# Kernel optimization log

Hardware: AMD Instinct MI355X
Metric: run time of the kernel (lower is better)

Reference implementation:

```python
import jax, jax.numpy as jnp
import numpy as np
from jax import lax

D = 1024      # dim
E = 2         # expand
DI = D * E    # d_inner = 2048
DS = 16       # d_state
DK = 3        # d_conv (3 so padding=1 preserves seq length)
DTR = 64      # dt_rank = ceil(dim/16)
B = 2
L = 4096


def setup_inputs() -> dict:
    key = jax.random.key(0)
    ks = jax.random.split(key, 8)
    s = 0.02
    return {
        "x": jax.random.normal(ks[0], (B, L, D), jnp.float32),
        "W_in": jax.random.normal(ks[1], (D, 2 * DI), jnp.float32) * s,
        "W_conv": jax.random.normal(ks[2], (DI, 1, DK), jnp.float32) * s,
        "W_xproj": jax.random.normal(ks[3], (DI, DTR + 2 * DS), jnp.float32) * s,
        "W_dt": jax.random.normal(ks[4], (DTR, DI), jnp.float32) * s,
        "b_dt": jax.random.normal(ks[5], (DI,), jnp.float32) * s,
        "W_out": jax.random.normal(ks[6], (DI, D), jnp.float32) * s,
        "ln_g": jnp.ones((DI,), jnp.float32),
        "ln_b": jnp.zeros((DI,), jnp.float32),
    }


def _silu(v):
    return v * jax.nn.sigmoid(v)


def _forward(x, W_in, W_conv, W_xproj, W_dt, b_dt, W_out, ln_g, ln_b):
    # in_proj and gate split
    xz = x @ W_in                                   # (B,L,2*DI)
    xs, z = jnp.split(xz, 2, axis=-1)               # (B,L,DI) each
    # depthwise conv1d (groups = DI), padding preserves L
    xc = lax.conv_general_dilated(
        xs.transpose(0, 2, 1), W_conv, (1,), [(DK // 2, DK // 2)],
        dimension_numbers=("NCH", "OIH", "NCH"), feature_group_count=DI)
    xs = _silu(xc.transpose(0, 2, 1))               # (B,L,DI)
    # x_proj -> dt, B, C
    xp = xs @ W_xproj                               # (B,L,DTR+2*DS)
    dt_lo = xp[..., :DTR]
    Bp = xp[..., DTR:DTR + DS]                      # (B,L,DS)
    Cp = xp[..., DTR + DS:]                         # (B,L,DS)
    dt = jax.nn.softplus(dt_lo @ W_dt + b_dt)       # (B,L,DI)
    # simplified selective scan: scalar decay/input per (b,t)
    dtm = dt.mean(-1)                               # (B,L)
    xm = xs.mean(-1)                                # (B,L)
    decay = jnp.exp(-dtm)                           # (B,L)
    Bx = Bp * xm[..., None]                         # (B,L,DS)

    def step(h, inp):
        d, bx = inp                                 # d:(B,), bx:(B,DS)
        h = h * d[:, None] + bx
        return h, h.sum(-1)                         # emit sum_s h[b,s]

    h0 = jnp.zeros((x.shape[0], DS), x.dtype)
    _, S = lax.scan(step, h0, (decay.T, Bx.transpose(1, 0, 2)))  # S:(L,B)
    y = Cp * S.T[..., None]                         # (B,L,DS): y_t = C_t * sum_s h_t
    y = jnp.tile(y, (1, 1, DI // DS))               # broadcast up to d_inner
    # LayerNorm(d_inner)
    mu = y.mean(-1, keepdims=True)
    var = y.var(-1, keepdims=True)
    y = (y - mu) * lax.rsqrt(var + 1e-5) * ln_g + ln_b
    # gate and out_proj
    y = y * _silu(z)
    return y @ W_out                                # (B,L,D)


def reference(x, W_in, W_conv, W_xproj, W_dt, b_dt, W_out, ln_g, ln_b):
    return _forward(x, W_in, W_conv, W_xproj, W_dt, b_dt, W_out, ln_g, ln_b)
```

## Files before the change

### kernel.cpp

```cpp
#include <hip/hip_runtime.h>
#include <hip/hip_bf16.h>
#include <math.h>
#include <stdint.h>

#define D_    1024
#define DI_   2048
#define DS_   16
#define DTR_  64
#define B_    2
#define L_    4096
#define ROWS_ 8192
#define NXZ_  4096

typedef __attribute__((ext_vector_type(8))) __bf16 bf16x8;
typedef __attribute__((ext_vector_type(4))) float  f32x4;

__device__ __forceinline__ unsigned short f2bf(float f) {
    unsigned u = __float_as_uint(f);
    unsigned r = (u + 0x7fffu + ((u >> 16) & 1u)) >> 16;
    return (unsigned short)r;
}
__device__ __forceinline__ float bf2f(unsigned short h) {
    return __uint_as_float(((unsigned)h) << 16);
}

__device__ __forceinline__ void gload16(const void* gp, void* lp) {
    auto* g1 = (const __attribute__((address_space(1))) unsigned int*)(uintptr_t)gp;
    auto* l3 = (__attribute__((address_space(3))) unsigned int*)(uintptr_t)lp;
    __builtin_amdgcn_global_load_lds(g1, l3, 16, 0, 0);
}

__global__ __launch_bounds__(256) void kcvt(const float* __restrict__ in,
                                            unsigned short* __restrict__ out) {
    const int i = blockIdx.x * 256 + threadIdx.x;
    const float4 v = ((const float4*)in)[i];
    ushort4 o;
    o.x = f2bf(v.x); o.y = f2bf(v.y); o.z = f2bf(v.z); o.w = f2bf(v.w);
    ((ushort4*)out)[i] = o;
}

__global__ __launch_bounds__(256) void ktrans(const float* __restrict__ W,
                                              unsigned short* __restrict__ WT,
                                              int R, int Csrc) {
    __shared__ float tile[32][33];
    const int c0 = blockIdx.x * 32, r0 = blockIdx.y * 32;
    const int tc = threadIdx.x & 31, tr = threadIdx.x >> 5;
#pragma unroll
    for (int i = 0; i < 32; i += 8)
        tile[tr + i][tc] = (c0 + tc < Csrc)
                           ? W[(size_t)(r0 + tr + i) * Csrc + c0 + tc] : 0.f;
    __syncthreads();
#pragma unroll
    for (int i = 0; i < 32; i += 8)
        WT[(size_t)(c0 + tr + i) * R + r0 + tc] = f2bf(tile[tc][tr + i]);
}

template <int K, bool BF16OUT>
__global__ __launch_bounds__(256, 3) void gemm_bf16(const unsigned short* __restrict__ A,
                                                    const unsigned short* __restrict__ B,
                                                    void* __restrict__ Cp, int ldc) {
    const int t    = threadIdx.x;
    const int wid  = t >> 6, lane = t & 63;
    const int gx  = gridDim.x;
    const int nwg = gx * gridDim.y;
    int lin = blockIdx.y * gx + blockIdx.x;
    lin = (lin & 7) * (nwg >> 3) + (lin >> 3);
    const int bx = lin % gx;
    const int nb = lin / gx;
    const int m0 = bx * 128;
    const int n0 = nb * 128;
    const int wr = wid >> 1, wc = wid & 1;
    __shared__ unsigned short Als[128 * 64];
    __shared__ unsigned short Bls[128 * 64];

    f32x4 acc[4][4];
    const f32x4 z4 = {0.f, 0.f, 0.f, 0.f};
#pragma unroll
    for (int m = 0; m < 4; ++m)
#pragma unroll
        for (int n = 0; n < 4; ++n) acc[m][n] = z4;

    int rowA[4], eoff[4];
#pragma unroll
    for (int i = 0; i < 4; ++i) {
        const int c = wid * 256 + i * 64 + lane;
        rowA[i] = c >> 3;
        eoff[i] = (c & 7) * 8;
    }

    const int ar = wr * 64 + (lane & 15);
    const int br = wc * 64 + (lane & 15);
    const int kq = (lane >> 4) * 8;

    for (int k0 = 0; k0 < K; k0 += 64) {
#pragma unroll
        for (int i = 0; i < 4; ++i) {
            const int dst = (wid * 4 + i) * 1024;
            gload16(A + (size_t)(m0 + rowA[i]) * K + k0 + eoff[i], (char*)Als + dst);
            gload16(B + (size_t)(n0 + rowA[i]) * K + k0 + eoff[i], (char*)Bls + dst);
        }
        __syncthreads();
        bf16x8 af[4][2], bfr[4][2];
#pragma unroll
        for (int m = 0; m < 4; ++m)
#pragma unroll
            for (int kk = 0; kk < 2; ++kk)
                af[m][kk] = *(const bf16x8*)&Als[(ar + m * 16) * 64 + kk * 32 + kq];
#pragma unroll
        for (int n = 0; n < 4; ++n)
#pragma unroll
            for (int kk = 0; kk < 2; ++kk)
                bfr[n][kk] = *(const bf16x8*)&Bls[(br + n * 16) * 64 + kk * 32 + kq];
#pragma unroll
        for (int m = 0; m < 4; ++m)
#pragma unroll
            for (int n = 0; n < 4; ++n)
#pragma unroll
                for (int kk = 0; kk < 2; ++kk)
                    acc[m][n] = __builtin_amdgcn_mfma_f32_16x16x32_bf16(
                        af[m][kk], bfr[n][kk], acc[m][n], 0, 0, 0);
        __syncthreads();
    }

    const int crow = (lane >> 4) * 4, ccol = lane & 15;
#pragma unroll
    for (int m = 0; m < 4; ++m)
#pragma unroll
        for (int n = 0; n < 4; ++n)
#pragma unroll
            for (int j = 0; j < 4; ++j) {
                const size_t idx = (size_t)(m0 + wr * 64 + m * 16 + crow + j) * ldc +
                                   (n0 + wc * 64 + n * 16 + ccol);
                if (BF16OUT) ((unsigned short*)Cp)[idx] = f2bf(acc[m][n][j]);
                else         ((float*)Cp)[idx] = acc[m][n][j];
            }
}

__global__ __launch_bounds__(256) void k2_conv(const unsigned short* __restrict__ xz,
                                               const float* __restrict__ Wcv,
                                               unsigned short* __restrict__ xsb,
                                               float* __restrict__ xm) {
    const int t = threadIdx.x;
    const int wid = t >> 6, lane = t & 63;
    const int row0 = blockIdx.x * 16;
    const int c0 = t * 8;
    __shared__ float wsum[16][4];
    float w0[8], w1[8], w2[8];
#pragma unroll
    for (int j = 0; j < 8; ++j) {
        w0[j] = Wcv[(c0 + j) * 3 + 0];
        w1[j] = Wcv[(c0 + j) * 3 + 1];
        w2[j] = Wcv[(c0 + j) * 3 + 2];
    }
    for (int r = 0; r < 16; ++r) {
        const int row = row0 + r;
        const int l = row & (L_ - 1);
        const unsigned short* cur = xz + (size_t)row * NXZ_ + c0;
        float cv[8], pv[8] = {}, nv[8] = {};
        {
            const uint4 raw = *(const uint4*)cur;
            const unsigned short* p = (const unsigned short*)&raw;
#pragma unroll
            for (int j = 0; j < 8; ++j) cv[j] = bf2f(p[j]);
        }
        if (l > 0) {
            const uint4 raw = *(const uint4*)(cur - NXZ_);
            const unsigned short* p = (const unsigned short*)&raw;
#pragma unroll
            for (int j = 0; j < 8; ++j) pv[j] = bf2f(p[j]);
        }
        if (l < L_ - 1) {
            const uint4 raw = *(const uint4*)(cur + NXZ_);
            const unsigned short* p = (const unsigned short*)&raw;
#pragma unroll
            for (int j = 0; j < 8; ++j) nv[j] = bf2f(p[j]);
        }
        float s8 = 0.f;
        unsigned short o[8];
#pragma unroll
        for (int j = 0; j < 8; ++j) {
            const float v = cv[j] * w1[j] + pv[j] * w0[j] + nv[j] * w2[j];
            const float s = v / (1.f + expf(-v));
            o[j] = f2bf(s);
            s8 += s;
        }
        *(uint4*)(xsb + (size_t)row * DI_ + c0) = *(const uint4*)o;
#pragma unroll
        for (int k = 1; k < 64; k <<= 1) s8 += __shfl_xor(s8, k);
        if (lane == 0) wsum[r][wid] = s8;
    }
    __syncthreads();
    if (t < 16)
        xm[row0 + t] = (wsum[t][0] + wsum[t][1] + wsum[t][2] + wsum[t][3]) * (1.f / (float)DI_);
}

__global__ __launch_bounds__(256, 2) void k3m(const unsigned short* __restrict__ A,
                                              const unsigned short* __restrict__ B,
                                              float* __restrict__ part) {
    const int t = threadIdx.x;
    const int wid = t >> 6, lane = t & 63;
    const int m0 = blockIdx.x * 128;
    const int kc = blockIdx.y;
    const int wr = wid >> 1, wc = wid & 1;
    __shared__ unsigned short Als[128 * 64];
    __shared__ unsigned short Bls[128 * 64];
    f32x4 acc[4][4];
    const f32x4 z4 = {0.f, 0.f, 0.f, 0.f};
#pragma unroll
    for (int m = 0; m < 4; ++m)
#pragma unroll
        for (int n = 0; n < 4; ++n) acc[m][n] = z4;
    int rowA[4], eoff[4];
#pragma unroll
    for (int i = 0; i < 4; ++i) {
        const int c = wid * 256 + i * 64 + lane;
        rowA[i] = c >> 3;
        eoff[i] = (c & 7) * 8;
    }
    const int ar = wr * 64 + (lane & 15);
    const int br = wc * 64 + (lane & 15);
    const int kq = (lane >> 4) * 8;
    const int kbase = kc * 512;
    for (int k0 = kbase; k0 < kbase + 512; k0 += 64) {
#pragma unroll
        for (int i = 0; i < 4; ++i) {
            const int dst = (wid * 4 + i) * 1024;
            gload16(A + (size_t)(m0 + rowA[i]) * DI_ + k0 + eoff[i], (char*)Als + dst);
            gload16(B + (size_t)rowA[i] * DI_ + k0 + eoff[i], (char*)Bls + dst);
        }
        __syncthreads();
        bf16x8 af[4][2], bfr[4][2];
#pragma unroll
        for (int m = 0; m < 4; ++m)
#pragma unroll
            for (int kk = 0; kk < 2; ++kk)
                af[m][kk] = *(const bf16x8*)&Als[(ar + m * 16) * 64 + kk * 32 + kq];
#pragma unroll
        for (int n = 0; n < 4; ++n)
#pragma unroll
            for (int kk = 0; kk < 2; ++kk)
                bfr[n][kk] = *(const bf16x8*)&Bls[(br + n * 16) * 64 + kk * 32 + kq];
#pragma unroll
        for (int m = 0; m < 4; ++m)
#pragma unroll
            for (int n = 0; n < 4; ++n)
#pragma unroll
                for (int kk = 0; kk < 2; ++kk)
                    acc[m][n] = __builtin_amdgcn_mfma_f32_16x16x32_bf16(
                        af[m][kk], bfr[n][kk], acc[m][n], 0, 0, 0);
        __syncthreads();
    }
    const int crow = (lane >> 4) * 4, ccol = lane & 15;
#pragma unroll
    for (int m = 0; m < 4; ++m)
#pragma unroll
        for (int n = 0; n < 4; ++n) {
            const int col = wc * 64 + n * 16 + ccol;
            if (col < 96) {
#pragma unroll
                for (int j = 0; j < 4; ++j)
                    part[((size_t)kc * ROWS_ + m0 + wr * 64 + m * 16 + crow + j) * 96 + col] =
                        acc[m][n][j];
            }
        }
}

__global__ __launch_bounds__(256) void kred(const float* __restrict__ part,
                                            float* __restrict__ xp,
                                            unsigned short* __restrict__ dtlo) {
    const int i = blockIdx.x * 256 + threadIdx.x;
    const size_t stride = (size_t)ROWS_ * 96 / 4;
    const float4* p = (const float4*)part;
    float4 a = p[i], b = p[i + stride], c = p[i + 2 * stride], d = p[i + 3 * stride];
    float4 o;
    o.x = a.x + b.x + c.x + d.x;
    o.y = a.y + b.y + c.y + d.y;
    o.z = a.z + b.z + c.z + d.z;
    o.w = a.w + b.w + c.w + d.w;
    ((float4*)xp)[i] = o;
    const int c4 = i % 24, row = i / 24;
    if (c4 < 16) {
        ushort4 h;
        h.x = f2bf(o.x); h.y = f2bf(o.y); h.z = f2bf(o.z); h.w = f2bf(o.w);
        *(ushort4*)(dtlo + (size_t)row * 64 + c4 * 4) = h;
    }
}

__global__ __launch_bounds__(256, 2) void k4m(const unsigned short* __restrict__ A,
                                              const unsigned short* __restrict__ B,
                                              const float* __restrict__ bdt,
                                              float* __restrict__ psum) {
    const int t = threadIdx.x;
    const int wid = t >> 6, lane = t & 63;
    const int m0 = blockIdx.x * 128;
    const int nb = blockIdx.y;
    const int wr = wid >> 1, wc = wid & 1;
    __shared__ unsigned short Als[128 * 64];
    __shared__ unsigned short Bls[128 * 64];
    __shared__ float srow[128][2];
    f32x4 acc[4][4];
    const f32x4 z4 = {0.f, 0.f, 0.f, 0.f};
#pragma unroll
    for (int m = 0; m < 4; ++m)
#pragma unroll
        for (int n = 0; n < 4; ++n) acc[m][n] = z4;
#pragma unroll
    for (int i = 0; i < 4; ++i) {
        const int c = wid * 256 + i * 64 + lane;
        const int row = c >> 3, eo = (c & 7) * 8;
        const int dst = (wid * 4 + i) * 1024;
        gload16(A + (size_t)(m0 + row) * 64 + eo, (char*)Als + dst);
        gload16(B + (size_t)(nb * 128 + row) * 64 + eo, (char*)Bls + dst);
    }
    __syncthreads();
    const int ar = wr * 64 + (lane & 15);
    const int br = wc * 64 + (lane & 15);
    const int kq = (lane >> 4) * 8;
    const int ccol = lane & 15;
    {
        bf16x8 af[4][2], bfr[4][2];
#pragma unroll
        for (int m = 0; m < 4; ++m)
#pragma unroll
            for (int kk = 0; kk < 2; ++kk)
                af[m][kk] = *(const bf16x8*)&Als[(ar + m * 16) * 64 + kk * 32 + kq];
#pragma unroll
        for (int n = 0; n < 4; ++n)
#pragma unroll
            for (int kk = 0; kk < 2; ++kk)
                bfr[n][kk] = *(const bf16x8*)&Bls[(br + n * 16) * 64 + kk * 32 + kq];
#pragma unroll
        for (int m = 0; m < 4; ++m)
#pragma unroll
            for (int n = 0; n < 4; ++n)
#pragma unroll
                for (int kk = 0; kk < 2; ++kk)
                    acc[m][n] = __builtin_amdgcn_mfma_f32_16x16x32_bf16(
                        af[m][kk], bfr[n][kk], acc[m][n], 0, 0, 0);
    }
    float bcol[4];
#pragma unroll
    for (int n = 0; n < 4; ++n) bcol[n] = bdt[nb * 128 + wc * 64 + n * 16 + ccol];
#pragma unroll
    for (int m = 0; m < 4; ++m)
#pragma unroll
        for (int j = 0; j < 4; ++j) {
            float s = 0.f;
#pragma unroll
            for (int n = 0; n < 4; ++n) {
                const float w = acc[m][n][j] + bcol[n];
                s += fmaxf(w, 0.f) + log1pf(expf(-fabsf(w)));
            }
#pragma unroll
            for (int mask = 1; mask < 16; mask <<= 1) s += __shfl_xor(s, mask);
            if (ccol == 0)
                srow[wr * 64 + m * 16 + (lane >> 4) * 4 + j][wc] = s;
        }
    __syncthreads();
    if (t < 128)
        psum[(size_t)nb * ROWS_ + m0 + t] = srow[t][0] + srow[t][1];
}

__global__ __launch_bounds__(256) void k4r(const float* __restrict__ psum,
                                           const float* __restrict__ xp,
                                           const float* __restrict__ xm,
                                           float* __restrict__ dec,
                                           float* __restrict__ u) {
    const int row = blockIdx.x * 256 + threadIdx.x;
    float tot = 0.f;
#pragma unroll
    for (int j = 0; j < 16; ++j) tot += psum[(size_t)j * ROWS_ + row];
    const float dtm = tot * (1.f / (float)DI_);
    float sBp = 0.f;
#pragma unroll
    for (int s = 0; s < DS_; ++s) sBp += xp[(size_t)row * 96 + DTR_ + s];
    dec[row] = expf(-dtm);
    u[row]   = xm[row] * sBp;
}

__global__ __launch_bounds__(256) void k5_scan(const float* __restrict__ dec,
                                               const float* __restrict__ u,
                                               float* __restrict__ S) {
    const int t = threadIdx.x;
    __shared__ float aa[256], hh[256], init[256];
    const int b = t >> 7, c = t & 127;
    const int base = b * L_ + c * 32;
    float a = 1.f, h = 0.f;
    for (int i = 0; i < 32; ++i) {
        const float d = dec[base + i];
        h = h * d + u[base + i];
        a *= d;
    }
    aa[t] = a; hh[t] = h;
    __syncthreads();
    if (t < B_) {
        float run = 0.f;
        for (int cc = 0; cc < 128; ++cc) {
            const int tt = t * 128 + cc;
            init[tt] = run;
            run = hh[tt] + aa[tt] * run;
        }
    }
    __syncthreads();
    h = init[t];
    for (int i = 0; i < 32; ++i) {
        h = h * dec[base + i] + u[base + i];
        S[base + i] = h;
    }
}

__global__ __launch_bounds__(256) void k6_v16(const float* __restrict__ xp,
                                              const float* __restrict__ S,
                                              float* __restrict__ v16) {
    const int row = blockIdx.x * 256 + threadIdx.x;
    const float s = S[row];
    float v[16], mu = 0.f;
#pragma unroll
    for (int i = 0; i < 16; ++i) {
        v[i] = xp[(size_t)row * 96 + DTR_ + DS_ + i] * s;
        mu += v[i];
    }
    mu *= (1.f / 16.f);
    float var = 0.f;
#pragma unroll
    for (int i = 0; i < 16; ++i) {
        const float d = v[i] - mu;
        var += d * d;
    }
    var *= (1.f / 16.f);
    const float rs = rsqrtf(var + 1e-5f);
#pragma unroll
    for (int i = 0; i < 16; ++i) v16[(size_t)row * 16 + i] = (v[i] - mu) * rs;
}

__global__ __launch_bounds__(256) void kA7(const unsigned short* __restrict__ xz,
                                           const float* __restrict__ v16,
                                           const float* __restrict__ g,
                                           const float* __restrict__ bb,
                                           unsigned short* __restrict__ Abf) {
    const int row = blockIdx.x;
    const int t   = threadIdx.x;
    __shared__ float vrow[16];
    if (t < 16) vrow[t] = v16[row * 16 + t];
    __syncthreads();
    const int i0 = t * 8;
    const uint4 zraw = *(const uint4*)(xz + (size_t)row * NXZ_ + 2048 + i0);
    const unsigned short* zp = (const unsigned short*)&zraw;
    const float4 g0 = *(const float4*)(g + i0),  g1 = *(const float4*)(g + i0 + 4);
    const float4 b0 = *(const float4*)(bb + i0), b1 = *(const float4*)(bb + i0 + 4);
    const float gv[8] = {g0.x, g0.y, g0.z, g0.w, g1.x, g1.y, g1.z, g1.w};
    const float bv[8] = {b0.x, b0.y, b0.z, b0.w, b1.x, b1.y, b1.z, b1.w};
    unsigned short o[8];
#pragma unroll
    for (int j = 0; j < 8; ++j) {
        const int i = i0 + j;
        const float zf = bf2f(zp[j]);
        const float sz = zf / (1.f + expf(-zf));
        o[j] = f2bf((vrow[i & 15] * gv[j] + bv[j]) * sz);
    }
    *(uint4*)(Abf + (size_t)row * DI_ + i0) = *(const uint4*)o;
}

extern "C" void kernel_launch(void* const* d_in, const int* in_sizes, int n_in,
                              void* d_out, int out_size, void* d_ws, size_t ws_size,
                              hipStream_t stream) {
    const float* x    = (const float*)d_in[0];
    const float* Win  = (const float*)d_in[1];
    const float* Wcv  = (const float*)d_in[2];
    const float* Wxp  = (const float*)d_in[3];
    const float* Wdt  = (const float*)d_in[4];
    const float* bdt  = (const float*)d_in[5];
    const float* Wout = (const float*)d_in[6];
    const float* lng  = (const float*)d_in[7];
    const float* lnb  = (const float*)d_in[8];
    float* out = (float*)d_out;

    char* base = (char*)d_ws;
    unsigned short* xz_bf   = (unsigned short*)(base + 0);
    unsigned short* xsb     = (unsigned short*)(base + 67108864);
    unsigned short* xbf     = (unsigned short*)(base + 100663296);
    unsigned short* Abf     = (unsigned short*)(base + 100663296);
    unsigned short* WoutT   = (unsigned short*)(base + 134217728);
    unsigned short* WinT    = (unsigned short*)(base + 138412032);
    unsigned short* WxpT    = (unsigned short*)(base + 146800640);
    unsigned short* WdtT    = (unsigned short*)(base + 147324928);
    float*          xp_part = (float*)(base + 147587072);
    float*          xp      = (float*)(base + 160169984);
    unsigned short* dtlo    = (unsigned short*)(base + 163315712);
    float*          psum    = (float*)(base + 164364288);
    float*          xm      = (float*)(base + 164888576);
    float*          dec     = (float*)(base + 164921344);
    float*          u       = (float*)(base + 164954112);
    float*          S       = (float*)(base + 164986880);
    float*          v16     = (float*)(base + 165019648);

    kcvt<<<ROWS_ * D_ / 1024, 256, 0, stream>>>(x, xbf);
    ktrans<<<dim3(NXZ_ / 32, D_ / 32), 256, 0, stream>>>(Win, WinT, D_, NXZ_);
    ktrans<<<dim3(4, DI_ / 32), 256, 0, stream>>>(Wxp, WxpT, DI_, 96);
    ktrans<<<dim3(DI_ / 32, DTR_ / 32), 256, 0, stream>>>(Wdt, WdtT, DTR_, DI_);
    gemm_bf16<D_, true><<<dim3(ROWS_ / 128, NXZ_ / 128), 256, 0, stream>>>(
        xbf, WinT, xz_bf, NXZ_);
    ktrans<<<dim3(D_ / 32, DI_ / 32), 256, 0, stream>>>(Wout, WoutT, DI_, D_);
    k2_conv<<<ROWS_ / 16, 256, 0, stream>>>(xz_bf, Wcv, xsb, xm);
    k3m<<<dim3(ROWS_ / 128, 4), 256, 0, stream>>>(xsb, WxpT, xp_part);
    kred<<<ROWS_ * 96 / 4 / 256, 256, 0, stream>>>(xp_part, xp, dtlo);
    k4m<<<dim3(ROWS_ / 128, DI_ / 128), 256, 0, stream>>>(dtlo, WdtT, bdt, psum);
    k4r<<<ROWS_ / 256, 256, 0, stream>>>(psum, xp, xm, dec, u);
    k5_scan<<<1, 256, 0, stream>>>(dec, u, S);
    k6_v16<<<ROWS_ / 256, 256, 0, stream>>>(xp, S, v16);
    kA7<<<ROWS_, 256, 0, stream>>>(xz_bf, v16, lng, lnb, Abf);
    gemm_bf16<DI_, false><<<dim3(ROWS_ / 128, D_ / 128), 256, 0, stream>>>(
        Abf, WoutT, out, D_);
}
```

Baseline: 387.4 us.

## Replace in-projection GEMM with 256x256 double-buffered swizzled MFMA kernel

Adds a new 512-thread GEMM kernel using 256x256 output tiles, an XOR-swizzled LDS layout, and a double-buffered pipeline that interleaves global-to-LDS staging with MFMA quadrants under barriers and s_setprio. It is used for the x@W_in projection (8192x4096x1024) in place of the 128x128 single-buffered kernel. The aim is better data reuse per tile, fewer LDS bank conflicts, and overlap of memory loads with compute. In exchange it uses 128KB of LDS and a large accumulator register set at one workgroup per CU, and the hand-placed waitcnt and barrier scheduling is fragile.

```diff
diff --git a/kernel.cpp b/kernel.cpp
--- a/kernel.cpp
+++ b/kernel.cpp
@@ -53,6 +53,133 @@
 #pragma unroll
     for (int i = 0; i < 32; i += 8)
         WT[(size_t)(c0 + tr + i) * R + r0 + tc] = f2bf(tile[tc][tr + i]);
+}
+
+#define MFMA_Q(MB, NB)                                                          \
+    _Pragma("unroll")                                                           \
+    for (int m_ = 0; m_ < 4; ++m_) {                                            \
+        _Pragma("unroll")                                                       \
+        for (int n_ = 0; n_ < 2; ++n_) {                                        \
+            _Pragma("unroll")                                                   \
+            for (int kk_ = 0; kk_ < 2; ++kk_)                                   \
+                acc[MB + m_][NB + n_] = __builtin_amdgcn_mfma_f32_16x16x32_bf16( \
+                    a[m_][kk_], b[NB + n_][kk_], acc[MB + m_][NB + n_], 0, 0, 0);\
+        }                                                                       \
+    }
+
+#define KTILE(BUF, KT1, W1, KT2, W2, KT3, W3, KT4, W4, VMODE)                   \
+    _Pragma("unroll")                                                           \
+    for (int m_ = 0; m_ < 4; ++m_) { a[m_][0] = lda(BUF, m_, 0);                \
+                                     a[m_][1] = lda(BUF, m_, 1); }              \
+    _Pragma("unroll")                                                           \
+    for (int n_ = 0; n_ < 2; ++n_) { b[n_][0] = ldb(BUF, n_, 0);                \
+                                     b[n_][1] = ldb(BUF, n_, 1); }              \
+    stage_ht(KT1, W1);                                                          \
+    __builtin_amdgcn_s_barrier();                                               \
+    __builtin_amdgcn_s_setprio(1); MFMA_Q(0, 0); __builtin_amdgcn_s_setprio(0); \
+    __builtin_amdgcn_s_barrier();                                               \
+    _Pragma("unroll")                                                           \
+    for (int n_ = 2; n_ < 4; ++n_) { b[n_][0] = ldb(BUF, n_, 0);                \
+                                     b[n_][1] = ldb(BUF, n_, 1); }              \
+    stage_ht(KT2, W2);                                                          \
+    __builtin_amdgcn_s_barrier();                                               \
+    __builtin_amdgcn_s_setprio(1); MFMA_Q(0, 2); __builtin_amdgcn_s_setprio(0); \
+    __builtin_amdgcn_s_barrier();                                               \
+    _Pragma("unroll")                                                           \
+    for (int m_ = 0; m_ < 4; ++m_) { a[m_][0] = lda(BUF, 4 + m_, 0);            \
+                                     a[m_][1] = lda(BUF, 4 + m_, 1); }          \
+    stage_ht(KT3, W3);                                                          \
+    __builtin_amdgcn_s_barrier();                                               \
+    __builtin_amdgcn_s_setprio(1); MFMA_Q(4, 0); __builtin_amdgcn_s_setprio(0); \
+    __builtin_amdgcn_s_barrier();                                               \
+    stage_ht(KT4, W4);                                                          \
+    if ((VMODE) == 1) { asm volatile("s_waitcnt vmcnt(4)" ::: "memory"); }      \
+    if ((VMODE) == 2) { asm volatile("s_waitcnt vmcnt(0)" ::: "memory"); }      \
+    __builtin_amdgcn_s_barrier();                                               \
+    __builtin_amdgcn_s_setprio(1); MFMA_Q(4, 2); __builtin_amdgcn_s_setprio(0); \
+    __builtin_amdgcn_s_barrier();
+
+template <int K>
+__global__ __launch_bounds__(512, 1) void gemm256(const unsigned short* __restrict__ A,
+                                                  const unsigned short* __restrict__ Bm,
+                                                  unsigned short* __restrict__ C, int ldc) {
+    constexpr int NT = K / 64;
+    const int t = threadIdx.x;
+    const int wid = t >> 6, lane = t & 63;
+    const int l15 = lane & 15, g = lane >> 4;
+    const int gx = gridDim.x, nwg = gx * gridDim.y;
+    int lin = blockIdx.y * gx + blockIdx.x;
+    lin = (lin & 7) * (nwg >> 3) + (lin >> 3);
+    const int m0 = (lin % gx) * 256;
+    const int n0 = (lin / gx) * 256;
+    const int wr = wid >> 2, wc = wid & 3;
+
+    __shared__ unsigned short lds[65536];
+
+    int pr[2], ps[2];
+#pragma unroll
+    for (int j = 0; j < 2; ++j) {
+        const int p = (wid * 2 + j) * 64 + lane;
+        pr[j] = p >> 3;
+        ps[j] = (p & 7) ^ (pr[j] & 7);
+    }
+    auto stage_ht = [&](int kt, int which) {
+        if (kt >= NT) return;
+        const int buf = kt & 1;
+        const int half = which & 1;
+        const bool isB = which >= 2;
+        const unsigned short* src = isB ? Bm : A;
+        const int row0 = isB ? n0 : m0;
+        const int base_byte = (isB ? 65536 : 0) + buf * 32768 + half * 16384;
+#pragma unroll
+        for (int j = 0; j < 2; ++j)
+            gload16(src + (size_t)(row0 + half * 128 + pr[j]) * K + kt * 64 + ps[j] * 8,
+                    (char*)lds + base_byte + (wid * 2 + j) * 1024);
+    };
+    auto lda = [&](int buf, int m, int kk) -> bf16x8 {
+        const int R = wr * 128 + m * 16 + l15;
+        const int S = kk * 4 + g;
+        return *(const bf16x8*)&lds[buf * 16384 + R * 64 + ((S ^ (l15 & 7)) << 3)];
+    };
+    auto ldb = [&](int buf, int n, int kk) -> bf16x8 {
+        const int R = wc * 64 + n * 16 + l15;
+        const int S = kk * 4 + g;
+        return *(const bf16x8*)&lds[32768 + buf * 16384 + R * 64 + ((S ^ (l15 & 7)) << 3)];
+    };
+
+    f32x4 acc[8][4];
+    const f32x4 z4 = {0.f, 0.f, 0.f, 0.f};
+#pragma unroll
+    for (int m = 0; m < 8; ++m)
+#pragma unroll
+        for (int n = 0; n < 4; ++n) acc[m][n] = z4;
+    bf16x8 a[4][2], b[4][2];
+
+    stage_ht(0, 2); stage_ht(0, 0); stage_ht(0, 1); stage_ht(0, 3);
+    stage_ht(1, 2); stage_ht(1, 0);
+    asm volatile("s_waitcnt vmcnt(4)" ::: "memory");
+    __builtin_amdgcn_s_barrier();
+
+    for (int it = 0; it < NT / 2; ++it) {
+        const int c = 2 * it;
+        if (it < NT / 2 - 1) {
+            KTILE(0, c + 1, 1, c + 1, 3, c + 2, 2, c + 2, 0, 1)
+            KTILE(1, c + 2, 1, c + 2, 3, c + 3, 2, c + 3, 0, 1)
+        } else {
+            KTILE(0, c + 1, 1, c + 1, 3, NT, 2, NT, 0, 2)
+            KTILE(1, NT, 1, NT, 3, NT, 2, NT, 0, 0)
+        }
+    }
+
+    const int crow = g * 4;
+#pragma unroll
+    for (int m = 0; m < 8; ++m)
+#pragma unroll
+        for (int n = 0; n < 4; ++n)
+#pragma unroll
+            for (int j = 0; j < 4; ++j)
+                C[(size_t)(m0 + wr * 128 + m * 16 + crow + j) * ldc +
+                  (n0 + wc * 64 + n * 16 + l15)] = f2bf(acc[m][n][j]);
 }
 
 template <int K, bool BF16OUT>
@@ -87,7 +214,6 @@
         rowA[i] = c >> 3;
         eoff[i] = (c & 7) * 8;
     }
-
     const int ar = wr * 64 + (lane & 15);
     const int br = wc * 64 + (lane & 15);
     const int kq = (lane >> 4) * 8;
@@ -498,7 +624,7 @@
     ktrans<<<dim3(NXZ_ / 32, D_ / 32), 256, 0, stream>>>(Win, WinT, D_, NXZ_);
     ktrans<<<dim3(4, DI_ / 32), 256, 0, stream>>>(Wxp, WxpT, DI_, 96);
     ktrans<<<dim3(DI_ / 32, DTR_ / 32), 256, 0, stream>>>(Wdt, WdtT, DTR_, DI_);
-    gemm_bf16<D_, true><<<dim3(ROWS_ / 128, NXZ_ / 128), 256, 0, stream>>>(
+    gemm256<D_><<<dim3(ROWS_ / 256, NXZ_ / 256), 512, 0, stream>>>(
         xbf, WinT, xz_bf, NXZ_);
     ktrans<<<dim3(D_ / 32, DI_ / 32), 256, 0, stream>>>(Wout, WoutT, DI_, D_);
     k2_conv<<<ROWS_ / 16, 256, 0, stream>>>(xz_bf, Wcv, xsb, xm);
```

Result: slower. 722.6 us (+86.5%).

## Replace bf16 GEMM with 256x128 double-buffered, swizzled, phase-interleaved kernel

Applied to the files above, without the earlier changes.

Both large projection GEMMs move to a new kernel with 512 threads and a 256x128 output tile. It double-buffers K-tiles in LDS with manual vmcnt waits instead of syncthreads, XOR-swizzles LDS rows to avoid bank conflicts, and splits each iteration into four MFMA phases interleaved with loads and setprio. The aim is to hide global-load latency and raise MFMA utilisation. In exchange it uses much more LDS (96 KB), gives fewer workgroups for the out-projection grid (32x8), and depends on a delicate barrier/waitcnt schedule.

```diff
diff --git a/kernel.cpp b/kernel.cpp
--- a/kernel.cpp
+++ b/kernel.cpp
@@ -56,22 +56,50 @@
 }
 
 template <int K, bool BF16OUT>
-__global__ __launch_bounds__(256, 3) void gemm_bf16(const unsigned short* __restrict__ A,
-                                                    const unsigned short* __restrict__ B,
-                                                    void* __restrict__ Cp, int ldc) {
-    const int t    = threadIdx.x;
-    const int wid  = t >> 6, lane = t & 63;
-    const int gx  = gridDim.x;
-    const int nwg = gx * gridDim.y;
+__global__ __launch_bounds__(512, 2) void gemm256b(const unsigned short* __restrict__ A,
+                                                   const unsigned short* __restrict__ Bm,
+                                                   void* __restrict__ Cp, int ldc) {
+    constexpr int NT = K / 64;
+    const int t = threadIdx.x;
+    const int wid = t >> 6, lane = t & 63;
+    const int l15 = lane & 15, g = lane >> 4;
+    const int gx = gridDim.x, nwg = gx * gridDim.y;
     int lin = blockIdx.y * gx + blockIdx.x;
     lin = (lin & 7) * (nwg >> 3) + (lin >> 3);
-    const int bx = lin % gx;
-    const int nb = lin / gx;
-    const int m0 = bx * 128;
-    const int n0 = nb * 128;
+    const int m0 = (lin % gx) * 256;
+    const int n0 = (lin / gx) * 128;
     const int wr = wid >> 1, wc = wid & 1;
-    __shared__ unsigned short Als[128 * 64];
-    __shared__ unsigned short Bls[128 * 64];
+
+    __shared__ unsigned short lds[49152];
+
+    int pr[2], ps[2];
+#pragma unroll
+    for (int j = 0; j < 2; ++j) {
+        const int p = (wid * 2 + j) * 64 + lane;
+        pr[j] = p >> 3;
+        ps[j] = (p & 7) ^ (pr[j] & 7);
+    }
+    auto stage = [&](int kt, int which) {
+        if (kt >= NT) return;
+        const int buf = kt & 1;
+        const unsigned short* src = (which == 2) ? Bm : A;
+        const int row0 = (which == 2) ? n0 : (m0 + ((which == 1) ? 128 : 0));
+        const int base_byte = buf * 49152 + which * 16384;
+#pragma unroll
+        for (int j = 0; j < 2; ++j)
+            gload16(src + (size_t)(row0 + pr[j]) * K + kt * 64 + ps[j] * 8,
+                    (char*)lds + base_byte + (wid * 2 + j) * 1024);
+    };
+    auto lda = [&](int buf, int m, int kk) -> bf16x8 {
+        const int R = wr * 64 + m * 16 + l15;
+        const int S = kk * 4 + g;
+        return *(const bf16x8*)&lds[buf * 24576 + R * 64 + ((S ^ (l15 & 7)) << 3)];
+    };
+    auto ldb = [&](int buf, int n, int kk) -> bf16x8 {
+        const int R = wc * 64 + n * 16 + l15;
+        const int S = kk * 4 + g;
+        return *(const bf16x8*)&lds[buf * 24576 + 16384 + R * 64 + ((S ^ (l15 & 7)) << 3)];
+    };
 
     f32x4 acc[4][4];
     const f32x4 z4 = {0.f, 0.f, 0.f, 0.f};
@@ -79,50 +107,78 @@
     for (int m = 0; m < 4; ++m)
 #pragma unroll
         for (int n = 0; n < 4; ++n) acc[m][n] = z4;
-
-    int rowA[4], eoff[4];
-#pragma unroll
-    for (int i = 0; i < 4; ++i) {
-        const int c = wid * 256 + i * 64 + lane;
-        rowA[i] = c >> 3;
-        eoff[i] = (c & 7) * 8;
-    }
-
-    const int ar = wr * 64 + (lane & 15);
-    const int br = wc * 64 + (lane & 15);
-    const int kq = (lane >> 4) * 8;
-
-    for (int k0 = 0; k0 < K; k0 += 64) {
-#pragma unroll
-        for (int i = 0; i < 4; ++i) {
-            const int dst = (wid * 4 + i) * 1024;
-            gload16(A + (size_t)(m0 + rowA[i]) * K + k0 + eoff[i], (char*)Als + dst);
-            gload16(B + (size_t)(n0 + rowA[i]) * K + k0 + eoff[i], (char*)Bls + dst);
-        }
-        __syncthreads();
-        bf16x8 af[4][2], bfr[4][2];
-#pragma unroll
-        for (int m = 0; m < 4; ++m)
-#pragma unroll
-            for (int kk = 0; kk < 2; ++kk)
-                af[m][kk] = *(const bf16x8*)&Als[(ar + m * 16) * 64 + kk * 32 + kq];
-#pragma unroll
-        for (int n = 0; n < 4; ++n)
-#pragma unroll
-            for (int kk = 0; kk < 2; ++kk)
-                bfr[n][kk] = *(const bf16x8*)&Bls[(br + n * 16) * 64 + kk * 32 + kq];
-#pragma unroll
-        for (int m = 0; m < 4; ++m)
-#pragma unroll
-            for (int n = 0; n < 4; ++n)
+    bf16x8 a[2][2], b[4][2];
+
+    stage(0, 0); stage(0, 1); stage(0, 2); stage(1, 0);
+    asm volatile("s_waitcnt vmcnt(2)" ::: "memory");
+    __builtin_amdgcn_s_barrier();
+
+    for (int it = 0; it < NT; ++it) {
+        const int buf = it & 1;
+#pragma unroll
+        for (int m = 0; m < 2; ++m) { a[m][0] = lda(buf, m, 0); a[m][1] = lda(buf, m, 1); }
+#pragma unroll
+        for (int n = 0; n < 2; ++n) { b[n][0] = ldb(buf, n, 0); b[n][1] = ldb(buf, n, 1); }
+        stage(it + 1, 1);
+        __builtin_amdgcn_s_barrier();
+        __builtin_amdgcn_s_setprio(1);
+#pragma unroll
+        for (int m = 0; m < 2; ++m)
+#pragma unroll
+            for (int n = 0; n < 2; ++n)
 #pragma unroll
                 for (int kk = 0; kk < 2; ++kk)
                     acc[m][n] = __builtin_amdgcn_mfma_f32_16x16x32_bf16(
-                        af[m][kk], bfr[n][kk], acc[m][n], 0, 0, 0);
-        __syncthreads();
-    }
-
-    const int crow = (lane >> 4) * 4, ccol = lane & 15;
+                        a[m][kk], b[n][kk], acc[m][n], 0, 0, 0);
+        __builtin_amdgcn_s_setprio(0);
+        __builtin_amdgcn_s_barrier();
+#pragma unroll
+        for (int n = 2; n < 4; ++n) { b[n][0] = ldb(buf, n, 0); b[n][1] = ldb(buf, n, 1); }
+        stage(it + 1, 2);
+        __builtin_amdgcn_s_barrier();
+        __builtin_amdgcn_s_setprio(1);
+#pragma unroll
+        for (int m = 0; m < 2; ++m)
+#pragma unroll
+            for (int n = 2; n < 4; ++n)
+#pragma unroll
+                for (int kk = 0; kk < 2; ++kk)
+                    acc[m][n] = __builtin_amdgcn_mfma_f32_16x16x32_bf16(
+                        a[m][kk], b[n][kk], acc[m][n], 0, 0, 0);
+        __builtin_amdgcn_s_setprio(0);
+        __builtin_amdgcn_s_barrier();
+#pragma unroll
+        for (int m = 0; m < 2; ++m) { a[m][0] = lda(buf, 2 + m, 0); a[m][1] = lda(buf, 2 + m, 1); }
+        __builtin_amdgcn_s_barrier();
+        __builtin_amdgcn_s_setprio(1);
+#pragma unroll
+        for (int m = 0; m < 2; ++m)
+#pragma unroll
+            for (int n = 0; n < 2; ++n)
+#pragma unroll
+                for (int kk = 0; kk < 2; ++kk)
+                    acc[2 + m][n] = __builtin_amdgcn_mfma_f32_16x16x32_bf16(
+                        a[m][kk], b[n][kk], acc[2 + m][n], 0, 0, 0);
+        __builtin_amdgcn_s_setprio(0);
+        __builtin_amdgcn_s_barrier();
+        stage(it + 2, 0);
+        if (it < NT - 2)       { asm volatile("s_waitcnt vmcnt(2)" ::: "memory"); }
+        else if (it == NT - 2) { asm volatile("s_waitcnt vmcnt(0)" ::: "memory"); }
+        __builtin_amdgcn_s_barrier();
+        __builtin_amdgcn_s_setprio(1);
+#pragma unroll
+        for (int m = 0; m < 2; ++m)
+#pragma unroll
+            for (int n = 2; n < 4; ++n)
+#pragma unroll
+                for (int kk = 0; kk < 2; ++kk)
+                    acc[2 + m][n] = __builtin_amdgcn_mfma_f32_16x16x32_bf16(
+                        a[m][kk], b[n][kk], acc[2 + m][n], 0, 0, 0);
+        __builtin_amdgcn_s_setprio(0);
+        __builtin_amdgcn_s_barrier();
+    }
+
+    const int crow = g * 4;
 #pragma unroll
     for (int m = 0; m < 4; ++m)
 #pragma unroll
@@ -130,7 +186,7 @@
 #pragma unroll
             for (int j = 0; j < 4; ++j) {
                 const size_t idx = (size_t)(m0 + wr * 64 + m * 16 + crow + j) * ldc +
-                                   (n0 + wc * 64 + n * 16 + ccol);
+                                   (n0 + wc * 64 + n * 16 + l15);
                 if (BF16OUT) ((unsigned short*)Cp)[idx] = f2bf(acc[m][n][j]);
                 else         ((float*)Cp)[idx] = acc[m][n][j];
             }
@@ -498,7 +554,7 @@
     ktrans<<<dim3(NXZ_ / 32, D_ / 32), 256, 0, stream>>>(Win, WinT, D_, NXZ_);
     ktrans<<<dim3(4, DI_ / 32), 256, 0, stream>>>(Wxp, WxpT, DI_, 96);
     ktrans<<<dim3(DI_ / 32, DTR_ / 32), 256, 0, stream>>>(Wdt, WdtT, DTR_, DI_);
-    gemm_bf16<D_, true><<<dim3(ROWS_ / 128, NXZ_ / 128), 256, 0, stream>>>(
+    gemm256b<D_, true><<<dim3(ROWS_ / 256, NXZ_ / 128), 512, 0, stream>>>(
         xbf, WinT, xz_bf, NXZ_);
     ktrans<<<dim3(D_ / 32, DI_ / 32), 256, 0, stream>>>(Wout, WoutT, DI_, D_);
     k2_conv<<<ROWS_ / 16, 256, 0, stream>>>(xz_bf, Wcv, xsb, xm);
@@ -509,6 +565,6 @@
     k5_scan<<<1, 256, 0, stream>>>(dec, u, S);
     k6_v16<<<ROWS_ / 256, 256, 0, stream>>>(xp, S, v16);
     kA7<<<ROWS_, 256, 0, stream>>>(xz_bf, v16, lng, lnb, Abf);
-    gemm_bf16<DI_, false><<<dim3(ROWS_ / 128, D_ / 128), 256, 0, stream>>>(
+    gemm256b<DI_, false><<<dim3(ROWS_ / 256, D_ / 128), 512, 0, stream>>>(
         Abf, WoutT, out, D_);
 }
```

After: 394.6 us. No clear change (+1.9%).
